# Kernel tuning notes

Measured on AMD Instinct MI355X. Metric: run time of the kernel, lower is better.

The kernel has to match this reference:

```python
import jax, jax.numpy as jnp
import numpy as np

B, NUM_ROIS, NUM_GT = 32, 8192, 128
NUM_SAMPLED = 512
POS_FRAC = 0.25
BACKGROUND = 0.0
VARIANCE = np.array([0.1, 0.1, 0.2, 0.2], np.float32)  # [dy, dx, dh, dw]
IMG = 1024.0


def _make_boxes(key, shape):
    # valid yxyx boxes: positive height/width, inside image
    kc, ks = jax.random.split(key)
    c = jax.random.uniform(kc, shape[:-1] + (2,), minval=0.2, maxval=0.8) * IMG
    hw = jax.random.uniform(ks, shape[:-1] + (2,), minval=0.05, maxval=0.3) * IMG
    return jnp.concatenate([c - 0.5 * hw, c + 0.5 * hw], axis=-1)


def setup_inputs() -> dict:
    key = jax.random.key(0)
    k1, k2, k3, k4 = jax.random.split(key, 4)
    rois = _make_boxes(k1, (B, NUM_ROIS, 4))
    gt_boxes = _make_boxes(k2, (B, NUM_GT, 4))
    gt_classes = jax.random.randint(k3, (B, NUM_GT, 1), 1, 81).astype(jnp.float32)
    # uniform noise used by balanced_sample (channel 0 for positives, 1 for negatives)
    sample_noise = jax.random.uniform(k4, (B, NUM_ROIS + NUM_GT, 2), dtype=jnp.float32)
    return {"rois": rois, "gt_boxes": gt_boxes, "gt_classes": gt_classes,
            "sample_noise": sample_noise}


def _compute_iou(a, b):
    # a: [B,N,4], b: [B,G,4] in yxyx; use_masking=True -> padded (-1) boxes get iou=-1
    a_ = a[:, :, None, :]   # [B,N,1,4]
    b_ = b[:, None, :, :]   # [B,1,G,4]
    iy = jnp.maximum(jnp.minimum(a_[..., 2], b_[..., 2]) - jnp.maximum(a_[..., 0], b_[..., 0]), 0.0)
    ix = jnp.maximum(jnp.minimum(a_[..., 3], b_[..., 3]) - jnp.maximum(a_[..., 1], b_[..., 1]), 0.0)
    inter = iy * ix
    area_a = (a[..., 2] - a[..., 0]) * (a[..., 3] - a[..., 1])  # [B,N]
    area_b = (b[..., 2] - b[..., 0]) * (b[..., 3] - b[..., 1])  # [B,G]
    union = area_a[:, :, None] + area_b[:, None, :] - inter
    iou = inter / jnp.maximum(union, 1e-8)
    mask_a = jnp.all(a == -1.0, axis=-1)  # [B,N] padded rois
    mask_b = jnp.all(b == -1.0, axis=-1)  # [B,G] padded gt
    masked = mask_a[:, :, None] | mask_b[:, None, :]
    return jnp.where(masked, -1.0, iou)


def _encode_deltas(anchors, boxes):
    # yxyx -> (dy,dx,dh,dw)/variance
    ah = anchors[..., 2] - anchors[..., 0]
    aw = anchors[..., 3] - anchors[..., 1]
    acy = anchors[..., 0] + 0.5 * ah
    acx = anchors[..., 1] + 0.5 * aw
    bh = boxes[..., 2] - boxes[..., 0]
    bw = boxes[..., 3] - boxes[..., 1]
    bcy = boxes[..., 0] + 0.5 * bh
    bcx = boxes[..., 1] + 0.5 * bw
    d = jnp.stack([(bcy - acy) / ah, (bcx - acx) / aw,
                   jnp.log(bh / ah), jnp.log(bw / aw)], axis=-1)
    return d / jnp.asarray(VARIANCE, d.dtype)


def _balanced_sample(pos, neg, noise, num_samples, pos_frac):
    # returns float indicator [B,N]: 1.0 for sampled rois
    num_pos = int(num_samples * pos_frac)
    num_neg = num_samples - num_pos
    b, n = pos.shape
    pos_scores = jnp.where(pos, noise[..., 0], -1.0)
    neg_scores = jnp.where(neg, noise[..., 1], -1.0)
    _, pi = jax.lax.top_k(pos_scores, num_pos)
    _, ni = jax.lax.top_k(neg_scores, num_neg)
    rows = jnp.arange(b)[:, None]
    # only mark picks that are actually positive/negative (handles scarcity)
    pv = jnp.take_along_axis(pos, pi, axis=-1).astype(jnp.float32)
    nv = jnp.take_along_axis(neg, ni, axis=-1).astype(jnp.float32)
    ind = jnp.zeros((b, n), jnp.float32)
    ind = ind.at[rows, pi].add(pv)
    ind = ind.at[rows, ni].add(nv)  # pos/neg disjoint -> stays in {0,1}
    return ind


def _gather(t, idx):
    # t: [B,M,D], idx: [B,K] -> [B,K,D]
    return jnp.take_along_axis(t, idx[..., None], axis=1)


def reference(rois, gt_boxes, gt_classes, sample_noise):
    # append_gt_boxes=True
    rois_all = jnp.concatenate([rois, gt_boxes], axis=1)  # [B, N+G, 4]
    sim = _compute_iou(rois_all, gt_boxes)                # [B, N+G, G]
    matched_cols = jnp.argmax(sim, axis=-1)               # [B, N+G]
    max_iou = jnp.max(sim, axis=-1)
    # ArgmaxBoxMatcher(thresholds=[0.0,0.5], match_values=[-2,-1,1])
    matched_vals = jnp.where(max_iou >= 0.5, 1, jnp.where(max_iou >= 0.0, -1, -2))
    positive = matched_vals == 1
    negative = matched_vals == -1
    background = ~positive                                # [B, N+G]

    matched_gt_classes = _gather(gt_classes, matched_cols)
    matched_gt_classes = jnp.where(background[..., None], BACKGROUND, matched_gt_classes)
    matched_gt_boxes = _gather(gt_boxes, matched_cols)
    encoded = _encode_deltas(rois_all, matched_gt_boxes)
    encoded = jnp.where(background[..., None], 0.0, encoded)

    indicators = _balanced_sample(positive, negative, sample_noise, NUM_SAMPLED, POS_FRAC)
    sampled_indicators, sampled_idx = jax.lax.top_k(indicators, NUM_SAMPLED)

    sampled_rois = _gather(rois_all, sampled_idx)
    sampled_gt_boxes = _gather(encoded, sampled_idx)
    sampled_gt_classes = _gather(matched_gt_classes, sampled_idx)
    sampled_box_weights = _gather(positive[..., None].astype(gt_boxes.dtype), sampled_idx)
    sampled_class_weights = sampled_indicators[..., None].astype(gt_classes.dtype)
    return (sampled_rois, sampled_gt_boxes, sampled_box_weights,
            sampled_gt_classes, sampled_class_weights)
```

## Files before the change

kernel.cpp:

```cpp
#include <hip/hip_runtime.h>
#include <cstdint>

#define NB 32
#define NROIS 8192
#define NGT 128
#define NALL (NROIS + NGT)
#define NSAMP 512
#define KPOS 128
#define KNEG 384
#define BCAP 1024
#define TS 1024
#define CH 9

__global__ __launch_bounds__(128) void k_match(
    const float* __restrict__ rois,
    const float* __restrict__ gt,
    const float* __restrict__ noise,
    int* __restrict__ mword)
{
  __shared__ float4 sg[NGT];
  __shared__ float sab[NGT];
  __shared__ unsigned long long smask[2];

  const int b = blockIdx.y;
  const int tid = threadIdx.x;
  const float4* gt4 = reinterpret_cast<const float4*>(gt) + (size_t)b * NGT;

  float4 g0 = gt4[tid];
  sg[tid] = g0;
  sab[tid] = (g0.z - g0.x) * (g0.w - g0.y);
  const bool mflag = (g0.x == -1.0f) && (g0.y == -1.0f) && (g0.z == -1.0f) && (g0.w == -1.0f);
  const unsigned long long mb = __ballot(mflag);
  if ((tid & 63) == 0) smask[tid >> 6] = mb;
  __syncthreads();
  const bool anymask = (smask[0] | smask[1]) != 0ULL;

  const int i = blockIdx.x * 128 + tid;
  float4 A = (blockIdx.x < 64)
    ? (reinterpret_cast<const float4*>(rois) + (size_t)b * NROIS)[i]
    : sg[tid];
  const float aar = (A.z - A.x) * (A.w - A.y);
  const bool ma = (A.x == -1.0f) && (A.y == -1.0f) && (A.z == -1.0f) && (A.w == -1.0f);

  int cc;
  int code;

  if (!anymask && __ballot(ma) == 0ULL) {
    float best[4];
    int bcol[4];
    #pragma unroll
    for (int c = 0; c < 4; ++c) { best[c] = -3.0e38f; bcol[c] = c * 32; }

    #pragma unroll 8
    for (int jj = 0; jj < 32; ++jj) {
      #pragma unroll
      for (int c = 0; c < 4; ++c) {
        const int j = c * 32 + jj;
        const float4 g = sg[j];
        float iy = fmaxf(fminf(A.z, g.z) - fmaxf(A.x, g.x), 0.0f);
        float ix = fmaxf(fminf(A.w, g.w) - fmaxf(A.y, g.y), 0.0f);
        float inter = iy * ix;
        float ab = (g.z - g.x) * (g.w - g.y);
        float uni = (aar + ab) - inter;
        float up = fmaxf(uni, 1e-8f);
        float r = __builtin_amdgcn_rcpf(up);
        r = r * (2.0f - up * r);
        float q = inter * r;
        if (q > best[c]) { best[c] = q; bcol[c] = j; }
      }
    }
    float bq = best[0]; cc = bcol[0];
    #pragma unroll
    for (int c = 1; c < 4; ++c) {
      if (best[c] > bq) { bq = best[c]; cc = bcol[c]; }
    }
    {
      #pragma clang fp contract(off)
      const float4 g = sg[cc];
      float iy = fmaxf(fminf(A.z, g.z) - fmaxf(A.x, g.x), 0.0f);
      float ix = fmaxf(fminf(A.w, g.w) - fmaxf(A.y, g.y), 0.0f);
      float inter = iy * ix;
      float ab = (g.z - g.x) * (g.w - g.y);
      float uni = (aar + ab) - inter;
      float bb = inter / fmaxf(uni, 1e-8f);
      code = (bb >= 0.5f) ? 3 : ((bb >= 0.0f) ? 1 : 0);
    }
  } else {
    #pragma clang fp contract(off)
    float bb = -3.0e38f; cc = 0;
    for (int j = 0; j < NGT; ++j) {
      float4 gg = sg[j];
      const bool mj = (gg.x == -1.0f) && (gg.y == -1.0f) && (gg.z == -1.0f) && (gg.w == -1.0f);
      float iy = fmaxf(fminf(A.z, gg.z) - fmaxf(A.x, gg.x), 0.0f);
      float ix = fmaxf(fminf(A.w, gg.w) - fmaxf(A.y, gg.y), 0.0f);
      float inter = iy * ix;
      float uni = (aar + sab[j]) - inter;
      float iou = inter / fmaxf(uni, 1e-8f);
      if (ma || mj) iou = -1.0f;
      if (iou > bb) { bb = iou; cc = j; }
    }
    code = (bb >= 0.5f) ? 3 : ((bb >= 0.0f) ? 1 : 0);
  }

  float2 nz = reinterpret_cast<const float2*>(noise)[(size_t)b * NALL + i];
  float v = (code == 3) ? nz.x : nz.y;
  int bin = (int)(v * 1024.0f);
  bin = bin < 0 ? 0 : (bin > 1023 ? 1023 : bin);
  mword[(size_t)b * NALL + i] = cc | (code << 7) | (bin << 9);
}

__device__ __forceinline__ int block_incl_scan(int v, int tid, int* wsum) {
  __syncthreads();
  int s = v;
  #pragma unroll
  for (int off = 1; off < 64; off <<= 1) {
    int u = __shfl_up(s, off);
    if ((tid & 63) >= off) s += u;
  }
  const int wid = tid >> 6;
  if ((tid & 63) == 63) wsum[wid] = s;
  __syncthreads();
  if (wid == 0) {
    const int lane = tid & 63;
    int w = (lane < (TS >> 6)) ? wsum[lane] : 0;
    #pragma unroll
    for (int off = 1; off < (TS >> 6); off <<= 1) {
      int u = __shfl_up(w, off);
      if (lane >= off) w += u;
    }
    if (lane < (TS >> 6)) wsum[lane] = w;
  }
  __syncthreads();
  return s + (wid ? wsum[wid - 1] : 0);
}

__global__ __launch_bounds__(TS) void k_select(
    const int* __restrict__ mword,
    const float* __restrict__ noise,
    const float* __restrict__ rois,
    const float* __restrict__ gt,
    const float* __restrict__ gtcls,
    float* __restrict__ out)
{
  #pragma clang fp contract(off)
  const int b = blockIdx.x;
  const int tid = threadIdx.x;

  __shared__ int hist[1024];
  __shared__ int wsum[TS >> 6];
  __shared__ int s_total;
  __shared__ float bval[2][BCAP];
  __shared__ int bidx_[2][BCAP];
  __shared__ int bcnt[2];
  __shared__ int s_bstar[2], s_need[2];
  __shared__ unsigned char ind[NALL];
  __shared__ unsigned short sorder[NSAMP];

  int ew[CH];

  hist[tid] = 0;
  if (tid < 2) bcnt[tid] = 0;

  #pragma unroll
  for (int k = 0; k < CH; ++k) {
    const int i = tid + k * TS;
    int w = 0;
    if (i < NALL) {
      ind[i] = 0;
      w = mword[(size_t)b * NALL + i];
    }
    ew[k] = w;
  }
  __syncthreads();
  #pragma unroll
  for (int k = 0; k < CH; ++k) {
    const int w = ew[k];
    if (w & 0x80) atomicAdd(&hist[w >> 9], (w & 0x100) ? 1 : (1 << 16));
  }
  __syncthreads();

  const int c = hist[tid];
  const int incl = block_incl_scan(c, tid, wsum);
  if (tid == TS - 1) s_total = incl;
  __syncthreads();
  const int total = s_total;

  #pragma unroll
  for (int p = 0; p < 2; ++p) {
    const int want = p ? KNEG : KPOS;
    const int sh = p ? 16 : 0;
    const int tot = (total >> sh) & 0xFFFF;
    if (tot >= want) {
      const int inc = (incl >> sh) & 0xFFFF;
      const int cp = (c >> sh) & 0xFFFF;
      const int above = tot - inc;
      if (above < want && above + cp >= want) {
        s_bstar[p] = tid; s_need[p] = want - above;
      }
    }
  }
  __syncthreads();

  const bool selall0 = ((total & 0xFFFF) < KPOS);
  const bool selall1 = (((total >> 16) & 0xFFFF) < KNEG);

  #pragma unroll
  for (int k = 0; k < CH; ++k) {
    const int w = ew[k];
    if (w & 0x80) {
      const int i = tid + k * TS;
      const int p = (w & 0x100) ? 0 : 1;
      const bool selall = p ? selall1 : selall0;
      const int bin = w >> 9;
      if (selall || bin > s_bstar[p]) {
        ind[i] = 1;
      } else if (bin == s_bstar[p]) {
        int pos = atomicAdd(&bcnt[p], 1);
        if (pos < BCAP) {
          bval[p][pos] = noise[((size_t)b * NALL + i) * 2 + p];
          bidx_[p][pos] = i;
        }
      }
    }
  }
  __syncthreads();

  #pragma unroll
  for (int p = 0; p < 2; ++p) {
    const bool selall = p ? selall1 : selall0;
    if (selall) continue;
    int cnt = bcnt[p]; if (cnt > BCAP) cnt = BCAP;
    const int need = s_need[p];
    for (int x = tid; x < cnt; x += TS) {
      const float v = bval[p][x];
      const int id = bidx_[p][x];
      int rank = 0;
      for (int y = 0; y < cnt; ++y) {
        const float vy = bval[p][y];
        const int iy2 = bidx_[p][y];
        rank += (vy > v) || (vy == v && iy2 < id);
      }
      if (rank < need) ind[id] = 1;
    }
  }
  __syncthreads();

  const int start = tid * CH;
  const int end = (start + CH < NALL) ? (start + CH) : NALL;
  int cnt1 = 0;
  for (int i = start; i < end; ++i) cnt1 += ind[i];
  const int incl1 = block_incl_scan(cnt1, tid, wsum);
  if (tid == TS - 1) s_total = incl1;
  __syncthreads();
  const int K1 = s_total;
  int ones_before = incl1 - cnt1;
  const int nzero = NSAMP - K1;
  for (int i = start; i < end; ++i) {
    if (ind[i]) {
      sorder[ones_before] = (unsigned short)i;
      ones_before++;
    } else {
      const int zrank = i - ones_before;
      if (zrank < nzero) sorder[K1 + zrank] = (unsigned short)i;
    }
  }
  __syncthreads();

  if (tid < NSAMP) {
    const int s = tid;
    const int idx = sorder[s];
    const size_t t = (size_t)b * NSAMP + s;

    float4 A = (idx < NROIS)
      ? reinterpret_cast<const float4*>(rois)[(size_t)b * NROIS + idx]
      : reinterpret_cast<const float4*>(gt)[(size_t)b * NGT + (idx - NROIS)];

    const int w = mword[(size_t)b * NALL + idx];
    const int col = w & 0x7F;
    const bool pos = (((w >> 7) & 3) == 3);

    float e0 = 0.f, e1 = 0.f, e2 = 0.f, e3 = 0.f, cls = 0.f;
    if (pos) {
      float4 G = reinterpret_cast<const float4*>(gt)[(size_t)b * NGT + col];
      float ah = A.z - A.x, aw = A.w - A.y;
      float acy = A.x + 0.5f * ah, acx = A.y + 0.5f * aw;
      float bh = G.z - G.x, bw = G.w - G.y;
      float bcy = G.x + 0.5f * bh, bcx = G.y + 0.5f * bw;
      e0 = ((bcy - acy) / ah) / 0.1f;
      e1 = ((bcx - acx) / aw) / 0.1f;
      e2 = logf(bh / ah) / 0.2f;
      e3 = logf(bw / aw) / 0.2f;
      cls = gtcls[(size_t)b * NGT + col];
    }

    float* o_rois = out;
    float* o_enc  = out + (size_t)NB * NSAMP * 4;
    float* o_bw   = out + (size_t)NB * NSAMP * 8;
    float* o_cls  = o_bw + (size_t)NB * NSAMP;
    float* o_cw   = o_cls + (size_t)NB * NSAMP;

    reinterpret_cast<float4*>(o_rois)[t] = A;
    float4 E; E.x = e0; E.y = e1; E.z = e2; E.w = e3;
    reinterpret_cast<float4*>(o_enc)[t] = E;
    o_bw[t]  = pos ? 1.0f : 0.0f;
    o_cls[t] = cls;
    o_cw[t]  = (s < K1) ? 1.0f : 0.0f;
  }
}

extern "C" void kernel_launch(void* const* d_in, const int* in_sizes, int n_in,
                              void* d_out, int out_size, void* d_ws, size_t ws_size,
                              hipStream_t stream) {
  const float* rois  = (const float*)d_in[0];
  const float* gt    = (const float*)d_in[1];
  const float* gtcls = (const float*)d_in[2];
  const float* noise = (const float*)d_in[3];
  float* out = (float*)d_out;

  int* mword = (int*)d_ws;

  dim3 g1(NALL / 128, NB);
  k_match<<<g1, 128, 0, stream>>>(rois, gt, noise, mword);
  k_select<<<NB, TS, 0, stream>>>(mword, noise, rois, gt, gtcls, out);
}
```

Baseline: 43.54 us.

## Process two ROIs per thread and compare IoU by cross-multiplication instead of division

The match kernel now has each thread handle two ROIs, halving the grid, so each shared-memory GT box load is reused for two IoU evaluations. The per-pair reciprocal plus Newton step is replaced by a division-free comparison that keeps the best intersection and union and compares by cross-multiplication. The exact IoU is still recomputed once for the chosen column. The aim is less shared-memory traffic and fewer transcendental ops per pair, at the cost of more registers and half as many waves. Ties or near-equal values may resolve differently than with true division.

```diff
diff --git a/kernel.cpp b/kernel.cpp
--- a/kernel.cpp
+++ b/kernel.cpp
@@ -5,6 +5,7 @@
 #define NROIS 8192
 #define NGT 128
 #define NALL (NROIS + NGT)
+#define NHALF (NALL / 2)
 #define NSAMP 512
 #define KPOS 128
 #define KNEG 384
@@ -25,6 +26,7 @@
   const int b = blockIdx.y;
   const int tid = threadIdx.x;
   const float4* gt4 = reinterpret_cast<const float4*>(gt) + (size_t)b * NGT;
+  const float4* rois4 = reinterpret_cast<const float4*>(rois) + (size_t)b * NROIS;
 
   float4 g0 = gt4[tid];
   sg[tid] = g0;
@@ -35,78 +37,141 @@
   __syncthreads();
   const bool anymask = (smask[0] | smask[1]) != 0ULL;
 
-  const int i = blockIdx.x * 128 + tid;
-  float4 A = (blockIdx.x < 64)
-    ? (reinterpret_cast<const float4*>(rois) + (size_t)b * NROIS)[i]
-    : sg[tid];
-  const float aar = (A.z - A.x) * (A.w - A.y);
-  const bool ma = (A.x == -1.0f) && (A.y == -1.0f) && (A.z == -1.0f) && (A.w == -1.0f);
-
-  int cc;
-  int code;
-
-  if (!anymask && __ballot(ma) == 0ULL) {
-    float best[4];
-    int bcol[4];
+  const int r = blockIdx.x * 128 + tid;
+  const bool act = (r < NHALF);
+  const int i1 = r;
+  const int i2 = r + NHALF;
+
+  float4 A1 = act ? rois4[i1] : rois4[0];
+  float4 A2 = act ? ((i2 < NROIS) ? rois4[i2] : sg[i2 - NROIS]) : rois4[0];
+  const float aar1 = (A1.z - A1.x) * (A1.w - A1.y);
+  const float aar2 = (A2.z - A2.x) * (A2.w - A2.y);
+  const bool ma1 = act && (A1.x == -1.0f) && (A1.y == -1.0f) && (A1.z == -1.0f) && (A1.w == -1.0f);
+  const bool ma2 = act && (A2.x == -1.0f) && (A2.y == -1.0f) && (A2.z == -1.0f) && (A2.w == -1.0f);
+
+  int cc1, cc2;
+  int code1, code2;
+
+  if (!anymask && __ballot(ma1 || ma2) == 0ULL) {
+    float bi1[4], bu1[4], bi2[4], bu2[4];
+    int bc1[4], bc2[4];
     #pragma unroll
-    for (int c = 0; c < 4; ++c) { best[c] = -3.0e38f; bcol[c] = c * 32; }
-
-    #pragma unroll 8
+    for (int c = 0; c < 4; ++c) {
+      bi1[c] = 0.0f; bu1[c] = 1.0f; bc1[c] = c * 32;
+      bi2[c] = 0.0f; bu2[c] = 1.0f; bc2[c] = c * 32;
+    }
+
+    #pragma unroll 4
     for (int jj = 0; jj < 32; ++jj) {
       #pragma unroll
       for (int c = 0; c < 4; ++c) {
         const int j = c * 32 + jj;
         const float4 g = sg[j];
-        float iy = fmaxf(fminf(A.z, g.z) - fmaxf(A.x, g.x), 0.0f);
-        float ix = fmaxf(fminf(A.w, g.w) - fmaxf(A.y, g.y), 0.0f);
+        const float ab = (g.z - g.x) * (g.w - g.y);
+        {
+          float iy = fmaxf(fminf(A1.z, g.z) - fmaxf(A1.x, g.x), 0.0f);
+          float ix = fmaxf(fminf(A1.w, g.w) - fmaxf(A1.y, g.y), 0.0f);
+          float inter = iy * ix;
+          float uc = fmaxf((aar1 + ab) - inter, 1e-8f);
+          const bool win = (inter * bu1[c]) > (bi1[c] * uc);
+          bi1[c] = win ? inter : bi1[c];
+          bu1[c] = win ? uc : bu1[c];
+          bc1[c] = win ? j : bc1[c];
+        }
+        {
+          float iy = fmaxf(fminf(A2.z, g.z) - fmaxf(A2.x, g.x), 0.0f);
+          float ix = fmaxf(fminf(A2.w, g.w) - fmaxf(A2.y, g.y), 0.0f);
+          float inter = iy * ix;
+          float uc = fmaxf((aar2 + ab) - inter, 1e-8f);
+          const bool win = (inter * bu2[c]) > (bi2[c] * uc);
+          bi2[c] = win ? inter : bi2[c];
+          bu2[c] = win ? uc : bu2[c];
+          bc2[c] = win ? j : bc2[c];
+        }
+      }
+    }
+    float qi = bi1[0], qu = bu1[0];
+    cc1 = bc1[0];
+    #pragma unroll
+    for (int c = 1; c < 4; ++c) {
+      const bool win = (bi1[c] * qu) > (qi * bu1[c]);
+      qi = win ? bi1[c] : qi; qu = win ? bu1[c] : qu; cc1 = win ? bc1[c] : cc1;
+    }
+    qi = bi2[0]; qu = bu2[0]; cc2 = bc2[0];
+    #pragma unroll
+    for (int c = 1; c < 4; ++c) {
+      const bool win = (bi2[c] * qu) > (qi * bu2[c]);
+      qi = win ? bi2[c] : qi; qu = win ? bu2[c] : qu; cc2 = win ? bc2[c] : cc2;
+    }
+    {
+      #pragma clang fp contract(off)
+      {
+        const float4 g = sg[cc1];
+        float iy = fmaxf(fminf(A1.z, g.z) - fmaxf(A1.x, g.x), 0.0f);
+        float ix = fmaxf(fminf(A1.w, g.w) - fmaxf(A1.y, g.y), 0.0f);
         float inter = iy * ix;
         float ab = (g.z - g.x) * (g.w - g.y);
-        float uni = (aar + ab) - inter;
-        float up = fmaxf(uni, 1e-8f);
-        float r = __builtin_amdgcn_rcpf(up);
-        r = r * (2.0f - up * r);
-        float q = inter * r;
-        if (q > best[c]) { best[c] = q; bcol[c] = j; }
-      }
-    }
-    float bq = best[0]; cc = bcol[0];
-    #pragma unroll
-    for (int c = 1; c < 4; ++c) {
-      if (best[c] > bq) { bq = best[c]; cc = bcol[c]; }
-    }
-    {
-      #pragma clang fp contract(off)
-      const float4 g = sg[cc];
-      float iy = fmaxf(fminf(A.z, g.z) - fmaxf(A.x, g.x), 0.0f);
-      float ix = fmaxf(fminf(A.w, g.w) - fmaxf(A.y, g.y), 0.0f);
-      float inter = iy * ix;
-      float ab = (g.z - g.x) * (g.w - g.y);
-      float uni = (aar + ab) - inter;
-      float bb = inter / fmaxf(uni, 1e-8f);
-      code = (bb >= 0.5f) ? 3 : ((bb >= 0.0f) ? 1 : 0);
+        float uni = (aar1 + ab) - inter;
+        float bb = inter / fmaxf(uni, 1e-8f);
+        code1 = (bb >= 0.5f) ? 3 : ((bb >= 0.0f) ? 1 : 0);
+      }
+      {
+        const float4 g = sg[cc2];
+        float iy = fmaxf(fminf(A2.z, g.z) - fmaxf(A2.x, g.x), 0.0f);
+        float ix = fmaxf(fminf(A2.w, g.w) - fmaxf(A2.y, g.y), 0.0f);
+        float inter = iy * ix;
+        float ab = (g.z - g.x) * (g.w - g.y);
+        float uni = (aar2 + ab) - inter;
+        float bb = inter / fmaxf(uni, 1e-8f);
+        code2 = (bb >= 0.5f) ? 3 : ((bb >= 0.0f) ? 1 : 0);
+      }
     }
   } else {
     #pragma clang fp contract(off)
-    float bb = -3.0e38f; cc = 0;
+    float bb1 = -3.0e38f, bb2 = -3.0e38f;
+    cc1 = 0; cc2 = 0;
     for (int j = 0; j < NGT; ++j) {
       float4 gg = sg[j];
       const bool mj = (gg.x == -1.0f) && (gg.y == -1.0f) && (gg.z == -1.0f) && (gg.w == -1.0f);
-      float iy = fmaxf(fminf(A.z, gg.z) - fmaxf(A.x, gg.x), 0.0f);
-      float ix = fmaxf(fminf(A.w, gg.w) - fmaxf(A.y, gg.y), 0.0f);
-      float inter = iy * ix;
-      float uni = (aar + sab[j]) - inter;
-      float iou = inter / fmaxf(uni, 1e-8f);
-      if (ma || mj) iou = -1.0f;
-      if (iou > bb) { bb = iou; cc = j; }
-    }
-    code = (bb >= 0.5f) ? 3 : ((bb >= 0.0f) ? 1 : 0);
-  }
-
-  float2 nz = reinterpret_cast<const float2*>(noise)[(size_t)b * NALL + i];
-  float v = (code == 3) ? nz.x : nz.y;
-  int bin = (int)(v * 1024.0f);
-  bin = bin < 0 ? 0 : (bin > 1023 ? 1023 : bin);
-  mword[(size_t)b * NALL + i] = cc | (code << 7) | (bin << 9);
+      {
+        float iy = fmaxf(fminf(A1.z, gg.z) - fmaxf(A1.x, gg.x), 0.0f);
+        float ix = fmaxf(fminf(A1.w, gg.w) - fmaxf(A1.y, gg.y), 0.0f);
+        float inter = iy * ix;
+        float uni = (aar1 + sab[j]) - inter;
+        float iou = inter / fmaxf(uni, 1e-8f);
+        if (ma1 || mj) iou = -1.0f;
+        if (iou > bb1) { bb1 = iou; cc1 = j; }
+      }
+      {
+        float iy = fmaxf(fminf(A2.z, gg.z) - fmaxf(A2.x, gg.x), 0.0f);
+        float ix = fmaxf(fminf(A2.w, gg.w) - fmaxf(A2.y, gg.y), 0.0f);
+        float inter = iy * ix;
+        float uni = (aar2 + sab[j]) - inter;
+        float iou = inter / fmaxf(uni, 1e-8f);
+        if (ma2 || mj) iou = -1.0f;
+        if (iou > bb2) { bb2 = iou; cc2 = j; }
+      }
+    }
+    code1 = (bb1 >= 0.5f) ? 3 : ((bb1 >= 0.0f) ? 1 : 0);
+    code2 = (bb2 >= 0.5f) ? 3 : ((bb2 >= 0.0f) ? 1 : 0);
+  }
+
+  if (act) {
+    {
+      float2 nz = reinterpret_cast<const float2*>(noise)[(size_t)b * NALL + i1];
+      float v = (code1 == 3) ? nz.x : nz.y;
+      int bin = (int)(v * 1024.0f);
+      bin = bin < 0 ? 0 : (bin > 1023 ? 1023 : bin);
+      mword[(size_t)b * NALL + i1] = cc1 | (code1 << 7) | (bin << 9);
+    }
+    {
+      float2 nz = reinterpret_cast<const float2*>(noise)[(size_t)b * NALL + i2];
+      float v = (code2 == 3) ? nz.x : nz.y;
+      int bin = (int)(v * 1024.0f);
+      bin = bin < 0 ? 0 : (bin > 1023 ? 1023 : bin);
+      mword[(size_t)b * NALL + i2] = cc2 | (code2 << 7) | (bin << 9);
+    }
+  }
 }
 
 __device__ __forceinline__ int block_incl_scan(int v, int tid, int* wsum) {
@@ -319,7 +384,7 @@
 
   int* mword = (int*)d_ws;
 
-  dim3 g1(NALL / 128, NB);
+  dim3 g1((NHALF + 127) / 128, NB);
   k_match<<<g1, 128, 0, stream>>>(rois, gt, noise, mword);
   k_select<<<NB, TS, 0, stream>>>(mword, noise, rois, gt, gtcls, out);
 }
```

Result: no change. 43.40 us (-0.3%).

## Spatially bin boxes and skip non-overlapping GT boxes per wave in matching

Applied to the files above, without the earlier changes.

Adds a pre-pass kernel that buckets all ROIs and GT boxes per image into a 16x16 grid by centre, producing a permuted index list. The match kernel then processes spatially coherent waves: it takes the union bounding box of each wave's boxes, ballots which GT boxes overlap it, and evaluates IoU only for those. The argmax comparison uses a division-free cross-multiplication. The exact IoU is still recomputed once for the winner. The cost is an extra kernel launch with only 32 blocks and atomic-based binning. Pruning may be weak because the boxes are large relative to the cells, and the serial mask loop has less instruction-level parallelism than the old unrolled loop.

```diff
diff --git a/kernel.cpp b/kernel.cpp
--- a/kernel.cpp
+++ b/kernel.cpp
@@ -11,69 +11,142 @@
 #define BCAP 1024
 #define TS 1024
 #define CH 9
-
-__global__ __launch_bounds__(128) void k_match(
+#define NWAVE (NALL / 64)
+
+__global__ __launch_bounds__(TS) void k_bin(
+    const float* __restrict__ rois,
+    const float* __restrict__ gt,
+    int* __restrict__ ridx)
+{
+  __shared__ int hist[256];
+  __shared__ int offs[256];
+  const int b = blockIdx.x;
+  const int tid = threadIdx.x;
+  const float4* rois4 = reinterpret_cast<const float4*>(rois) + (size_t)b * NROIS;
+  const float4* gt4 = reinterpret_cast<const float4*>(gt) + (size_t)b * NGT;
+
+  if (tid < 256) hist[tid] = 0;
+  __syncthreads();
+
+  int cells[CH];
+  #pragma unroll
+  for (int k = 0; k < CH; ++k) {
+    const int i = tid + k * TS;
+    int c = -1;
+    if (i < NALL) {
+      float4 A = (i < NROIS) ? rois4[i] : gt4[i - NROIS];
+      int cy = (int)((A.x + A.z) * (0.5f / 64.0f));
+      int cx = (int)((A.y + A.w) * (0.5f / 64.0f));
+      cy = cy < 0 ? 0 : (cy > 15 ? 15 : cy);
+      cx = cx < 0 ? 0 : (cx > 15 ? 15 : cx);
+      c = (cy << 4) | cx;
+      atomicAdd(&hist[c], 1);
+    }
+    cells[k] = c;
+  }
+  __syncthreads();
+
+  if (tid < 64) {
+    const int h0 = hist[4*tid], h1 = hist[4*tid+1], h2 = hist[4*tid+2], h3 = hist[4*tid+3];
+    int inc = h0 + h1 + h2 + h3;
+    const int s = inc;
+    #pragma unroll
+    for (int off = 1; off < 64; off <<= 1) {
+      int u = __shfl_up(inc, off);
+      if (tid >= off) inc += u;
+    }
+    const int excl = inc - s;
+    offs[4*tid]   = excl;
+    offs[4*tid+1] = excl + h0;
+    offs[4*tid+2] = excl + h0 + h1;
+    offs[4*tid+3] = excl + h0 + h1 + h2;
+  }
+  __syncthreads();
+
+  #pragma unroll
+  for (int k = 0; k < CH; ++k) {
+    if (cells[k] >= 0) {
+      const int p = atomicAdd(&offs[cells[k]], 1);
+      ridx[(size_t)b * NALL + p] = tid + k * TS;
+    }
+  }
+}
+
+__global__ __launch_bounds__(256) void k_match(
     const float* __restrict__ rois,
     const float* __restrict__ gt,
     const float* __restrict__ noise,
+    const int* __restrict__ ridx,
     int* __restrict__ mword)
 {
   __shared__ float4 sg[NGT];
   __shared__ float sab[NGT];
-  __shared__ unsigned long long smask[2];
+  __shared__ unsigned long long sgm[2];
 
   const int b = blockIdx.y;
   const int tid = threadIdx.x;
+  const int lane = tid & 63;
+  const int wv = tid >> 6;
   const float4* gt4 = reinterpret_cast<const float4*>(gt) + (size_t)b * NGT;
-
-  float4 g0 = gt4[tid];
-  sg[tid] = g0;
-  sab[tid] = (g0.z - g0.x) * (g0.w - g0.y);
-  const bool mflag = (g0.x == -1.0f) && (g0.y == -1.0f) && (g0.z == -1.0f) && (g0.w == -1.0f);
-  const unsigned long long mb = __ballot(mflag);
-  if ((tid & 63) == 0) smask[tid >> 6] = mb;
-  __syncthreads();
-  const bool anymask = (smask[0] | smask[1]) != 0ULL;
-
-  const int i = blockIdx.x * 128 + tid;
-  float4 A = (blockIdx.x < 64)
-    ? (reinterpret_cast<const float4*>(rois) + (size_t)b * NROIS)[i]
-    : sg[tid];
+  const float4* rois4 = reinterpret_cast<const float4*>(rois) + (size_t)b * NROIS;
+
+  if (tid < NGT) {
+    float4 g0 = gt4[tid];
+    sg[tid] = g0;
+    sab[tid] = (g0.z - g0.x) * (g0.w - g0.y);
+    const bool mflag = (g0.x == -1.0f) && (g0.y == -1.0f) && (g0.z == -1.0f) && (g0.w == -1.0f);
+    const unsigned long long mb = __ballot(mflag);
+    if (lane == 0) sgm[tid >> 6] = mb;
+  }
+  __syncthreads();
+  const bool anygt = (sgm[0] | sgm[1]) != 0ULL;
+
+  const int w = blockIdx.x * 4 + wv;
+  if (w >= NWAVE) return;
+  const int i = ridx[(size_t)b * NALL + w * 64 + lane];
+
+  float4 A = (i < NROIS) ? rois4[i] : sg[i - NROIS];
   const float aar = (A.z - A.x) * (A.w - A.y);
   const bool ma = (A.x == -1.0f) && (A.y == -1.0f) && (A.z == -1.0f) && (A.w == -1.0f);
+  const unsigned long long mam = __ballot(ma);
 
   int cc;
   int code;
 
-  if (!anymask && __ballot(ma) == 0ULL) {
-    float best[4];
-    int bcol[4];
+  if (!anygt && mam == 0ULL) {
+    float by0 = A.x, bx0 = A.y, by1 = A.z, bx1 = A.w;
     #pragma unroll
-    for (int c = 0; c < 4; ++c) { best[c] = -3.0e38f; bcol[c] = c * 32; }
-
-    #pragma unroll 8
-    for (int jj = 0; jj < 32; ++jj) {
-      #pragma unroll
-      for (int c = 0; c < 4; ++c) {
-        const int j = c * 32 + jj;
-        const float4 g = sg[j];
-        float iy = fmaxf(fminf(A.z, g.z) - fmaxf(A.x, g.x), 0.0f);
-        float ix = fmaxf(fminf(A.w, g.w) - fmaxf(A.y, g.y), 0.0f);
-        float inter = iy * ix;
-        float ab = (g.z - g.x) * (g.w - g.y);
-        float uni = (aar + ab) - inter;
-        float up = fmaxf(uni, 1e-8f);
-        float r = __builtin_amdgcn_rcpf(up);
-        r = r * (2.0f - up * r);
-        float q = inter * r;
-        if (q > best[c]) { best[c] = q; bcol[c] = j; }
-      }
-    }
-    float bq = best[0]; cc = bcol[0];
-    #pragma unroll
-    for (int c = 1; c < 4; ++c) {
-      if (best[c] > bq) { bq = best[c]; cc = bcol[c]; }
-    }
+    for (int off = 32; off >= 1; off >>= 1) {
+      by0 = fminf(by0, __shfl_xor(by0, off));
+      bx0 = fminf(bx0, __shfl_xor(bx0, off));
+      by1 = fmaxf(by1, __shfl_xor(by1, off));
+      bx1 = fmaxf(bx1, __shfl_xor(bx1, off));
+    }
+    const float4 gA = sg[lane];
+    const float4 gB = sg[lane + 64];
+    const bool ovA = (gA.x <= by1) && (gA.z >= by0) && (gA.y <= bx1) && (gA.w >= bx0);
+    const bool ovB = (gB.x <= by1) && (gB.z >= by0) && (gB.y <= bx1) && (gB.w >= bx0);
+    unsigned long long m0 = __ballot(ovA);
+    unsigned long long m1 = __ballot(ovB);
+
+    float bi = 0.0f, bS = 1.0f;
+    int bc = 0;
+    auto eval = [&](int j) {
+      const float4 g = sg[j];
+      const float ab = (g.z - g.x) * (g.w - g.y);
+      const float S = aar + ab;
+      float iy = fmaxf(fminf(A.z, g.z) - fmaxf(A.x, g.x), 0.0f);
+      float ix = fmaxf(fminf(A.w, g.w) - fmaxf(A.y, g.y), 0.0f);
+      float inter = iy * ix;
+      const bool win = (inter * bS) > (bi * S);
+      bi = win ? inter : bi;
+      bS = win ? S : bS;
+      bc = win ? j : bc;
+    };
+    while (m0) { const int j = __builtin_ctzll(m0); m0 &= m0 - 1; eval(j); }
+    while (m1) { const int j = 64 + __builtin_ctzll(m1); m1 &= m1 - 1; eval(j); }
+    cc = bc;
+
     {
       #pragma clang fp contract(off)
       const float4 g = sg[cc];
@@ -87,7 +160,8 @@
     }
   } else {
     #pragma clang fp contract(off)
-    float bb = -3.0e38f; cc = 0;
+    float bb = -3.0e38f;
+    cc = 0;
     for (int j = 0; j < NGT; ++j) {
       float4 gg = sg[j];
       const bool mj = (gg.x == -1.0f) && (gg.y == -1.0f) && (gg.z == -1.0f) && (gg.w == -1.0f);
@@ -317,9 +391,12 @@
   const float* noise = (const float*)d_in[3];
   float* out = (float*)d_out;
 
-  int* mword = (int*)d_ws;
-
-  dim3 g1(NALL / 128, NB);
-  k_match<<<g1, 128, 0, stream>>>(rois, gt, noise, mword);
+  uint8_t* ws = (uint8_t*)d_ws;
+  int* mword = (int*)ws;
+  int* ridx  = (int*)(ws + (size_t)NB * NALL * sizeof(int));
+
+  k_bin<<<NB, TS, 0, stream>>>(rois, gt, ridx);
+  dim3 g1((NWAVE + 3) / 4, NB);
+  k_match<<<g1, 256, 0, stream>>>(rois, gt, noise, ridx, mword);
   k_select<<<NB, TS, 0, stream>>>(mword, noise, rois, gt, gtcls, out);
 }
```

After: 46.85 us. 1.08x slower.
